# Kernel tuning notes

Measured on AMD Instinct MI355X. Metric: run time of the kernel, lower is better.

Reference implementation:

```python
import jax, jax.numpy as jnp
import numpy as np

N = 2048; E = 32768; E2 = 65536; B = 8; P = 20; M = B * P * P * P
NR = 16; SH = 9; FEAT = NR * SH; RE = 64; RH = 128; MC = 32; MH = 16; MODES = 10; CUT = 5.0


def _sh(u):
    # real spherical harmonics l=0,1,2, e3nn 'integral' normalization, on unit vectors u[...,3]
    x, y, z = u[..., 0], u[..., 1], u[..., 2]
    c0 = 0.28209479177387814  # 1/(2 sqrt(pi))
    c1 = 0.4886025119029199   # sqrt(3/(4 pi))
    l0 = jnp.full(x.shape, c0, dtype=u.dtype)
    return jnp.stack([
        l0,
        c1 * y, c1 * z, c1 * x,
        1.0925484305920792 * x * y,
        1.0925484305920792 * y * z,
        0.31539156525252005 * (3.0 * z * z - 1.0),
        1.0925484305920792 * x * z,
        0.5462742152960396 * (x * x - y * y),
    ], axis=-1)


def _gauss(r):
    # soft_one_hot_linspace(basis='gaussian', cutoff=False) * sqrt(RE)
    vals = jnp.linspace(0.0, CUT, RE)
    step = vals[1] - vals[0]
    d = (r[:, None] - vals) / step
    return jnp.exp(-d * d) / 1.12 * np.sqrt(RE)


def _norm_act(x):
    # NormActivation over irreps 16x0e + 16x1 + 16x2 (layout [16 | 16*3 | 16*5])
    s = x[:, :NR]
    v = x[:, NR:NR * 4].reshape(-1, NR, 3)
    t = x[:, NR * 4:].reshape(-1, NR, 5)
    s = s * jax.nn.sigmoid(jnp.abs(s))
    v = v * jax.nn.sigmoid(jnp.linalg.norm(v, axis=-1))[..., None]
    t = t * jax.nn.sigmoid(jnp.linalg.norm(t, axis=-1))[..., None]
    return jnp.concatenate([s, v.reshape(-1, NR * 3), t.reshape(-1, NR * 5)], axis=-1)


def _rmlp(e, m1, m2, m3):
    h = jax.nn.silu(e @ m1)
    h = jax.nn.silu(h @ m2)
    return h @ m3


def _gcn(src, dst, x, sh, emb_e, W, m1, m2, m3, n_dst, Wsc=None):
    # fully-connected tensor-product message passing: gather -> outer(feat, sh) -> GEMM
    # -> radial gate -> scatter-sum; optional self-connection
    xs = x[src]                                                    # [E, Cin]
    msg = (xs[:, :, None] * sh[:, None, :]).reshape(xs.shape[0], -1) @ W
    msg = msg * _rmlp(emb_e, m1, m2, m3)
    out = jax.ops.segment_sum(msg, dst, num_segments=n_dst)
    return out if Wsc is None else out + x @ Wsc


def _spec(x, wr, wi):
    # FNO-style 3D spectral conv on [B,P,P,P,C], low MODES kept in 4 corner blocks
    Px = x.shape[1]
    xf = jnp.fft.rfftn(x, axes=(1, 2, 3))
    w = wr + 1j * wi                                              # [4,C,C,m,m,m]
    m = MODES
    of = jnp.zeros(xf.shape, dtype=xf.dtype)
    corners = [(slice(0, m), slice(0, m)), (slice(-m, None), slice(0, m)),
               (slice(0, m), slice(-m, None)), (slice(-m, None), slice(-m, None))]
    for k, (s1, s2) in enumerate(corners):
        blk = jnp.einsum('bxyzi,ioxyz->bxyzo', xf[:, s1, s2, :m, :], w[k])
        of = of.at[:, s1, s2, :m, :].set(blk)
    return jnp.fft.irfftn(of, s=(Px, Px, Px), axes=(1, 2, 3))


def _forward(pos, cell, emb, g0_W, g0_Wsc, g0_m1, g0_m2, g0_m3,
             g12_W, g12_Wsc, g12_m1, g12_m2, g12_m3,
             a2m_W, a2m_m1, a2m_m2, a2m_m3,
             m2a_W, m2a_m1, m2a_m2, m2a_m3,
             fc0_W, fc0_b, sw_r, sw_i, pw, ff1, ff2, fc1, fc2,
             atomic_numbers, batch, edge_src, edge_dst, atom_src, mesh_dst):
    # atom-atom spherical GCN stack
    ev = pos[edge_src] - pos[edge_dst]
    el = jnp.linalg.norm(ev, axis=-1) + 1e-8
    sh_e = _sh(ev / el[:, None])
    emb_e = _gauss(el)
    x = emb[atomic_numbers]                                        # [N, NR]
    x = _gcn(edge_src, edge_dst, x, sh_e, emb_e, g0_W, g0_m1, g0_m2, g0_m3, N, g0_Wsc)
    for i in range(2):
        x = _norm_act(x)
        x = _gcn(edge_src, edge_dst, x, sh_e, emb_e, g12_W[i], g12_m1[i], g12_m2[i], g12_m3[i], N, g12_Wsc[i])
    # particle mesh positions per cell
    fr = jnp.arange(P) / P
    fg = jnp.stack(jnp.meshgrid(fr, fr, fr, indexing='ij'), axis=-1)   # [P,P,P,3]
    meshpos = jnp.einsum('xyzk,bkl->bxyzl', fg, cell).reshape(-1, 3)   # [M,3]
    # atom -> mesh conv
    ev2 = meshpos[mesh_dst] - pos[atom_src]
    el2 = jnp.linalg.norm(ev2, axis=-1) + 1e-8
    sh2 = _sh(ev2 / el2[:, None])
    emb2 = _gauss(el2)
    mf = _gcn(atom_src, mesh_dst, x, sh2, emb2, a2m_W, a2m_m1, a2m_m2, a2m_m3, M)   # [M, MC]
    mf = mf * jax.nn.sigmoid(jnp.abs(mf))                          # NormActivation on 0e
    mf = mf.reshape(B, P, P, P, MC)
    # PME / FNO mesh conv
    grid = jnp.broadcast_to(fg, (B, P, P, P, 3))
    h = jnp.concatenate([mf, grid], axis=-1) @ fc0_W + fc0_b       # lift to width MH
    for l in range(3):
        h = jax.nn.gelu(_spec(h, sw_r[l], sw_i[l]) + h @ pw[l])
        h = h + jax.nn.gelu(h @ ff1[l]) @ ff2[l]                   # using_ff branch
    h = jax.nn.gelu(h @ fc1) @ fc2                                 # [B,P,P,P,MH]
    mf2 = h.reshape(-1, MH)
    # mesh -> atom conv, per-atom energy, readout
    af = _gcn(mesh_dst, atom_src, mf2, sh2, emb2, m2a_W, m2a_m1, m2a_m2, m2a_m3, N)  # [N,1]
    return jax.ops.segment_sum(af, batch, num_segments=B)          # [B,1]


def setup_inputs():
    key = jax.random.key(0)
    ks = jax.random.split(key, 40)
    r = lambda i, shape, scale: jax.random.normal(ks[i], shape, dtype=jnp.float32) * scale
    inp = {}
    inp['pos'] = jax.random.uniform(ks[0], (N, 3), dtype=jnp.float32) * 10.0
    inp['cell'] = jnp.eye(3, dtype=jnp.float32)[None] * 10.0 + r(1, (B, 3, 3), 0.05)
    inp['atomic_numbers'] = jax.random.randint(ks[2], (N,), 1, 100)
    inp['batch'] = jnp.sort(jax.random.randint(ks[3], (N,), 0, B))
    inp['edge_src'] = jax.random.randint(ks[4], (E,), 0, N)
    inp['edge_dst'] = jax.random.randint(ks[5], (E,), 0, N)
    inp['atom_src'] = jax.random.randint(ks[6], (E2,), 0, N)
    inp['mesh_dst'] = jax.random.randint(ks[7], (E2,), 0, M)
    inp['emb'] = r(8, (100, NR), 1.0)
    inp['g0_W'] = r(9, (NR * SH, FEAT), (NR * SH) ** -0.5)
    inp['g0_Wsc'] = r(10, (NR, FEAT), NR ** -0.5)
    inp['g0_m1'] = r(11, (RE, RH), RE ** -0.5)
    inp['g0_m2'] = r(12, (RH, RH), RH ** -0.5)
    inp['g0_m3'] = r(13, (RH, FEAT), RH ** -0.5)
    inp['g12_W'] = r(14, (2, FEAT * SH, FEAT), (FEAT * SH) ** -0.5)
    inp['g12_Wsc'] = r(15, (2, FEAT, FEAT), FEAT ** -0.5)
    inp['g12_m1'] = r(16, (2, RE, RH), RE ** -0.5)
    inp['g12_m2'] = r(17, (2, RH, RH), RH ** -0.5)
    inp['g12_m3'] = r(18, (2, RH, FEAT), RH ** -0.5)
    inp['a2m_W'] = r(19, (FEAT * SH, MC), (FEAT * SH) ** -0.5)
    inp['a2m_m1'] = r(20, (RE, RH), RE ** -0.5)
    inp['a2m_m2'] = r(21, (RH, RH), RH ** -0.5)
    inp['a2m_m3'] = r(22, (RH, MC), RH ** -0.5)
    inp['m2a_W'] = r(23, (MH * SH, 1), (MH * SH) ** -0.5)
    inp['m2a_m1'] = r(24, (RE, RH), RE ** -0.5)
    inp['m2a_m2'] = r(25, (RH, RH), RH ** -0.5)
    inp['m2a_m3'] = r(26, (RH, 1), RH ** -0.5)
    inp['fc0_W'] = r(27, (MC + 3, MH), (MC + 3) ** -0.5)
    inp['fc0_b'] = jnp.zeros((MH,), dtype=jnp.float32)
    inp['sw_r'] = r(28, (3, 4, MH, MH, MODES, MODES, MODES), 1.0 / MH)
    inp['sw_i'] = r(29, (3, 4, MH, MH, MODES, MODES, MODES), 1.0 / MH)
    inp['pw'] = r(30, (3, MH, MH), MH ** -0.5)
    inp['ff1'] = r(31, (3, MH, 4 * MH), MH ** -0.5)
    inp['ff2'] = r(32, (3, 4 * MH, MH), (4 * MH) ** -0.5)
    inp['fc1'] = r(33, (MH, 128), MH ** -0.5)
    inp['fc2'] = r(34, (128, MH), 128 ** -0.5)
    return inp


def reference(pos, cell, emb, g0_W, g0_Wsc, g0_m1, g0_m2, g0_m3, g12_W, g12_Wsc, g12_m1, g12_m2, g12_m3, a2m_W, a2m_m1, a2m_m2, a2m_m3, m2a_W, m2a_m1, m2a_m2, m2a_m3, fc0_W, fc0_b, sw_r, sw_i, pw, ff1, ff2, fc1, fc2, atomic_numbers, batch, edge_src, edge_dst, atom_src, mesh_dst):
    return _forward(pos, cell, emb, g0_W, g0_Wsc, g0_m1, g0_m2, g0_m3, g12_W, g12_Wsc, g12_m1, g12_m2, g12_m3, a2m_W, a2m_m1, a2m_m2, a2m_m3, m2a_W, m2a_m1, m2a_m2, m2a_m3, fc0_W, fc0_b, sw_r, sw_i, pw, ff1, ff2, fc1, fc2, atomic_numbers, batch, edge_src, edge_dst, atom_src, mesh_dst)
```

## Files before the change

kernel.cpp:

```cpp
#include <hip/hip_runtime.h>
#include <math.h>

#define DEVI __device__ __forceinline__

namespace {

constexpr int N_  = 2048;
constexpr int E_  = 32768;
constexpr int E2_ = 65536;
constexpr int M_  = 64000;
constexpr int NT_ = 2048;
constexpr float TMAX_ = 5.5f;
constexpr float TH_ = TMAX_ / NT_;

using bf16x8 = __attribute__((ext_vector_type(8))) short;
using f32x4  = __attribute__((ext_vector_type(4))) float;

DEVI float sigm(float x)  { return 1.0f/(1.0f+expf(-x)); }
DEVI float geluf(float x) {
  float t = tanhf(0.7978845608028654f*(x + 0.044715f*x*x*x));
  return 0.5f*x*(1.0f+t);
}

DEVI unsigned short bf16rn(float x){
  unsigned u = __float_as_uint(x);
  unsigned r = u + 0x7FFFu + ((u>>16)&1u);
  return (unsigned short)(r>>16);
}
DEVI void bf16split(float x, unsigned short& h, unsigned short& l){
  h = bf16rn(x);
  float hf = __uint_as_float(((unsigned)h)<<16);
  l = bf16rn(x - hf);
}

__global__ void zero_k(float* __restrict__ p, int n){
  int i = blockIdx.x*256 + threadIdx.x;
  if (i < n) p[i] = 0.0f;
}

__global__ void meshpos_k(const float* __restrict__ cell, float* __restrict__ mp){
  int m = blockIdx.x*256 + threadIdx.x;
  if (m >= M_) return;
  int b = m/8000, r = m%8000;
  float fx = (float)(r/400)    * 0.05f;
  float fy = (float)((r/20)%20)* 0.05f;
  float fz = (float)(r%20)     * 0.05f;
  const float* c = cell + b*9;
  mp[(size_t)m*3+0] = fx*c[0] + fy*c[3] + fz*c[6];
  mp[(size_t)m*3+1] = fx*c[1] + fy*c[4] + fz*c[7];
  mp[(size_t)m*3+2] = fx*c[2] + fy*c[5] + fz*c[8];
}

__global__ void edge_geom2_k(const float* __restrict__ Ppos, const int* __restrict__ pi,
                             const float* __restrict__ Qpos, const int* __restrict__ qi,
                             float* __restrict__ sh, float* __restrict__ el_out, int nE){
  int e = blockIdx.x*256 + threadIdx.x;
  if (e >= nE) return;
  int a = pi[e], b = qi[e];
  float ex = Ppos[(size_t)a*3+0] - Qpos[(size_t)b*3+0];
  float ey = Ppos[(size_t)a*3+1] - Qpos[(size_t)b*3+1];
  float ez = Ppos[(size_t)a*3+2] - Qpos[(size_t)b*3+2];
  float el = sqrtf(ex*ex+ey*ey+ez*ez) + 1e-8f;
  el_out[e] = el;
  float x = ex/el, y = ey/el, z = ez/el;
  float* s = sh + (size_t)e*9;
  s[0] = 0.28209479177387814f;
  s[1] = 0.4886025119029199f*y;
  s[2] = 0.4886025119029199f*z;
  s[3] = 0.4886025119029199f*x;
  s[4] = 1.0925484305920792f*x*y;
  s[5] = 1.0925484305920792f*y*z;
  s[6] = 0.31539156525252005f*(3.0f*z*z-1.0f);
  s[7] = 1.0925484305920792f*x*z;
  s[8] = 0.5462742152960396f*(x*x-y*y);
}

__global__ void gather_emb_k(const float* __restrict__ emb, const int* __restrict__ an,
                             float* __restrict__ x16){
  int idx = blockIdx.x*256 + threadIdx.x;
  if (idx >= N_*16) return;
  int n = idx >> 4, f = idx & 15;
  x16[idx] = emb[(size_t)an[n]*16 + f];
}

__global__ void es_k(float* __restrict__ Es){
  int idx = blockIdx.x*256 + threadIdx.x;
  if (idx >= NT_*64) return;
  int r = idx >> 6, k = idx & 63;
  const float step = 5.0f/63.0f;
  float d = (r*TH_ - k*step)/step;
  Es[idx] = expf(-d*d)*(8.0f/1.12f);
}

DEVI float lerp_tab(const float* __restrict__ T, float el, int O, int o){
  float u = el * (1.0f/TH_);
  u = fminf(u, (float)(NT_-1));
  int i = (int)u; if (i > NT_-2) i = NT_-2;
  float f = u - (float)i;
  float t0 = T[(size_t)i*O + o];
  float t1 = T[(size_t)(i+1)*O + o];
  return t0 + f*(t1 - t0);
}

struct BG {
  const float* A[5]; const float* B[5]; float* C[5];
  int K; int Nc[5];
};
template<int ACT>
__global__ __launch_bounds__(256) void bgemm_k(BG args){
  int chain = blockIdx.z;
  const float* A = args.A[chain];
  const float* Bm = args.B[chain];
  float* C = args.C[chain];
  int K = args.K, Nc = args.Nc[chain];
  int row0 = blockIdx.y*64, col0 = blockIdx.x*64;
  if (col0 >= Nc) return;
  __shared__ float As[16][72];
  __shared__ float Bs[16][72];
  int tid = threadIdx.x;
  int tx = tid & 15, ty = tid >> 4;
  float acc[4][4] = {};
  for (int k0 = 0; k0 < K; k0 += 16) {
    { int kk = tid & 15; int mloc = tid >> 4;
      int gk = k0 + kk;
      #pragma unroll
      for (int p = 0; p < 4; ++p) {
        int m = mloc + p*16; int gm = row0 + m;
        As[kk][m] = A[(size_t)gm*K + gk];
      } }
    { int nn = tid & 63; int kl = tid >> 6;
      #pragma unroll
      for (int p = 0; p < 4; ++p) {
        int kk = kl + p*4; int gk = k0 + kk; int gn = col0 + nn;
        Bs[kk][nn] = (gn < Nc) ? Bm[(size_t)gk*Nc + gn] : 0.0f;
      } }
    __syncthreads();
    #pragma unroll
    for (int kk = 0; kk < 16; ++kk) {
      float4 a4 = *(const float4*)&As[kk][ty*4];
      float4 b4 = *(const float4*)&Bs[kk][tx*4];
      float a[4] = {a4.x,a4.y,a4.z,a4.w};
      float b[4] = {b4.x,b4.y,b4.z,b4.w};
      #pragma unroll
      for (int i=0;i<4;++i)
        #pragma unroll
        for (int j=0;j<4;++j) acc[i][j] += a[i]*b[j];
    }
    __syncthreads();
  }
  for (int i=0;i<4;++i) {
    int gm = row0 + ty*4+i;
    for (int j=0;j<4;++j) {
      int gn = col0 + tx*4+j; if (gn >= Nc) continue;
      float v = acc[i][j];
      if (ACT==1) v = v*sigm(v);
      C[(size_t)gm*Nc + gn] = v;
    }
  }
}

__global__ void convA_k(const float* __restrict__ x, unsigned short* __restrict__ hi,
                        unsigned short* __restrict__ lo, int Mr, int K, int KP){
  int idx = blockIdx.x*256 + threadIdx.x;
  if (idx >= Mr*KP) return;
  int n = idx / KP, k = idx - n*KP;
  unsigned short h = 0, l = 0;
  if (k < K) bf16split(x[(size_t)n*K + k], h, l);
  hi[idx] = h; lo[idx] = l;
}

__global__ void convT_k(const float* __restrict__ B, unsigned short* __restrict__ hi,
                        unsigned short* __restrict__ lo, int K, int Nc, int KP){
  int idx = blockIdx.x*256 + threadIdx.x;
  if (idx >= Nc*KP) return;
  int n = idx / KP, k = idx - n*KP;
  unsigned short h = 0, l = 0;
  if (k < K) bf16split(B[(size_t)k*Nc + n], h, l);
  hi[idx] = h; lo[idx] = l;
}

template<int O>
__global__ void wreshapeT_k(const float* __restrict__ W, unsigned short* __restrict__ hi,
                            unsigned short* __restrict__ lo, int F, int KP){
  int idx = blockIdx.x*256 + threadIdx.x;
  int total = 9*O*KP;
  if (idx >= total) return;
  int n = idx / KP, f = idx - n*KP;
  unsigned short h = 0, l = 0;
  if (f < F){
    int s = n / O, o = n - s*O;
    bf16split(W[(size_t)(f*9+s)*O + o], h, l);
  }
  hi[idx] = h; lo[idx] = l;
}

__global__ void normact_bf_k(const float* __restrict__ x, unsigned short* __restrict__ hi,
                             unsigned short* __restrict__ lo){
  int idx = blockIdx.x*256 + threadIdx.x;
  if (idx >= N_*16) return;
  int n = idx >> 4, r = idx & 15;
  const float* xr = x + (size_t)n*144;
  unsigned short* hr = hi + (size_t)n*160;
  unsigned short* lr = lo + (size_t)n*160;
  unsigned short h, l;
  float s = xr[r];
  bf16split(s * sigm(fabsf(s)), h, l); hr[r]=h; lr[r]=l;
  float v0 = xr[16+r*3], v1 = xr[16+r*3+1], v2 = xr[16+r*3+2];
  float gv = sigm(sqrtf(v0*v0+v1*v1+v2*v2));
  bf16split(v0*gv,h,l); hr[16+r*3]=h;   lr[16+r*3]=l;
  bf16split(v1*gv,h,l); hr[16+r*3+1]=h; lr[16+r*3+1]=l;
  bf16split(v2*gv,h,l); hr[16+r*3+2]=h; lr[16+r*3+2]=l;
  float t0=xr[64+r*5],t1=xr[64+r*5+1],t2=xr[64+r*5+2],t3=xr[64+r*5+3],t4=xr[64+r*5+4];
  float gt = sigm(sqrtf(t0*t0+t1*t1+t2*t2+t3*t3+t4*t4));
  bf16split(t0*gt,h,l); hr[64+r*5]=h;   lr[64+r*5]=l;
  bf16split(t1*gt,h,l); hr[64+r*5+1]=h; lr[64+r*5+1]=l;
  bf16split(t2*gt,h,l); hr[64+r*5+2]=h; lr[64+r*5+2]=l;
  bf16split(t3*gt,h,l); hr[64+r*5+3]=h; lr[64+r*5+3]=l;
  bf16split(t4*gt,h,l); hr[64+r*5+4]=h; lr[64+r*5+4]=l;
  hr[144+r] = 0; lr[144+r] = 0;
}

__global__ __launch_bounds__(256) void mgemm_k(const unsigned short* __restrict__ Ah,
                     const unsigned short* __restrict__ Al,
                     const unsigned short* __restrict__ BTh,
                     const unsigned short* __restrict__ Bl,
                     float* __restrict__ C, int Mr, int KP, int Nc){
  int tilesN = Nc >> 4;
  int wid = ((blockIdx.x*256 + threadIdx.x) >> 6);
  int tm = wid / tilesN, tn = wid - tm*tilesN;
  if (tm*16 >= Mr) return;
  int lane = threadIdx.x & 63;
  int l15 = lane & 15;
  int kb  = (lane >> 4) * 8;
  const unsigned short* ah = Ah + (size_t)(tm*16 + l15)*KP + kb;
  const unsigned short* al = Al + (size_t)(tm*16 + l15)*KP + kb;
  const unsigned short* bh = BTh + (size_t)(tn*16 + l15)*KP + kb;
  const unsigned short* bl = Bl  + (size_t)(tn*16 + l15)*KP + kb;
  f32x4 acc = {0.f,0.f,0.f,0.f};
  for (int k0 = 0; k0 < KP; k0 += 32) {
    bf16x8 a_h = *(const bf16x8*)(ah + k0);
    bf16x8 a_l = *(const bf16x8*)(al + k0);
    bf16x8 b_h = *(const bf16x8*)(bh + k0);
    bf16x8 b_l = *(const bf16x8*)(bl + k0);
    acc = __builtin_amdgcn_mfma_f32_16x16x32_bf16(a_h, b_h, acc, 0, 0, 0);
    acc = __builtin_amdgcn_mfma_f32_16x16x32_bf16(a_h, b_l, acc, 0, 0, 0);
    acc = __builtin_amdgcn_mfma_f32_16x16x32_bf16(a_l, b_h, acc, 0, 0, 0);
  }
  int r0 = tm*16 + (lane>>4)*4;
  int co = tn*16 + l15;
  #pragma unroll
  for (int r = 0; r < 4; ++r){
    C[(size_t)(r0+r)*Nc + co] = acc[r];
  }
}

template<int O>
__global__ void econtract_k(const float* __restrict__ Y, const int* __restrict__ src,
                            const int* __restrict__ dst, const float* __restrict__ SH,
                            const float* __restrict__ EL, const float* __restrict__ T,
                            float* __restrict__ out, int nE){
  int idx = blockIdx.x*256 + threadIdx.x;
  if (idx >= nE*O) return;
  int e = idx / O, o = idx - e*O;
  const float* sr = SH + (size_t)e*9;
  const float* yr = Y + (size_t)src[e]*(9*O) + o;
  float acc = 0.0f;
  #pragma unroll
  for (int s = 0; s < 9; ++s) acc += sr[s] * yr[s*O];
  float rv = lerp_tab(T, EL[e], O, o);
  atomicAdd(&out[(size_t)dst[e]*O + o], acc * rv);
}

__global__ void fc0_k(const float* __restrict__ mf, const float* __restrict__ Wt,
                      const float* __restrict__ bb, float* __restrict__ h){
  int idx = blockIdx.x*256 + threadIdx.x;
  if (idx >= M_*16) return;
  int m = idx >> 4, o = idx & 15;
  int r = m % 8000;
  float fx = (float)(r/400)*0.05f, fy = (float)((r/20)%20)*0.05f, fz = (float)(r%20)*0.05f;
  const float* mfr = mf + (size_t)m*32;
  float acc = bb[o];
  #pragma unroll
  for (int j=0;j<32;++j){
    float v = mfr[j];
    v = v * sigm(fabsf(v));
    acc += v*Wt[j*16+o];
  }
  acc += fx*Wt[32*16+o] + fy*Wt[33*16+o] + fz*Wt[34*16+o];
  h[idx] = acc;
}

__global__ __launch_bounds__(256) void wreorder2_k(const float* __restrict__ wr, const float* __restrict__ wi,
                          float2* __restrict__ W2){
  __shared__ float2 tile[2560];
  int l = blockIdx.y;
  const float* wrl = wr + (size_t)l*1024000;
  const float* wil = wi + (size_t)l*1024000;
  int p = blockIdx.x;
  int ky = p/20, kx = p%20;
  int corner = ((kx>=10)?1:0) + ((ky>=10)?2:0);
  int base2 = corner*256;
  int soff = (kx%10)*100 + (ky%10)*10;
  for (int t = threadIdx.x; t < 2560; t += 256){
    int chunk = t/10, kz = t - chunk*10;
    size_t src = (size_t)(base2 + chunk)*1000 + soff + kz;
    tile[kz*256 + chunk] = make_float2(wrl[src], wil[src]);
  }
  __syncthreads();
  float2* dst = W2 + (size_t)l*1024000 + (size_t)p*2560;
  for (int t = threadIdx.x; t < 2560; t += 256) dst[t] = tile[t];
}

__global__ __launch_bounds__(256) void zyfwd_k(const float* __restrict__ h, float2* __restrict__ cA){
  __shared__ float  pl[20][20][4];
  __shared__ float2 tz[20][10][4];
  __shared__ float2 tw[20];
  int tid = threadIdx.x;
  if (tid < 20){ float a = -6.283185307179586f*tid/20.0f; tw[tid] = make_float2(cosf(a), sinf(a)); }
  int bid = blockIdx.x;
  int b = bid / 80, rem = bid % 80;
  int X = rem >> 2, cg = rem & 3;
  const float* hp = h + (size_t)(b*20+X)*400*16 + cg*4;
  for (int t = tid; t < 400; t += 256) {
    int y = t/20, z = t%20;
    const float4 v = *(const float4*)(hp + (size_t)t*16);
    pl[y][z][0]=v.x; pl[y][z][1]=v.y; pl[y][z][2]=v.z; pl[y][z][3]=v.w;
  }
  __syncthreads();
  for (int t = tid; t < 800; t += 256) {
    int c = t & 3, kz = (t>>2)%10, y = t/40;
    float sr=0.0f, si=0.0f; int j=0;
    for (int z=0; z<20; ++z){
      float v = pl[y][z][c];
      float2 w = tw[j];
      sr += v*w.x; si += v*w.y;
      j += kz; if (j>=20) j-=20;
    }
    tz[y][kz][c] = make_float2(sr,si);
  }
  __syncthreads();
  for (int t = tid; t < 800; t += 256) {
    int c = t & 3, kz = (t>>2)%10, ky = t/40;
    float sr=0.0f, si=0.0f; int j=0;
    for (int y=0; y<20; ++y){
      float2 v = tz[y][kz][c];
      float2 w = tw[j];
      sr += v.x*w.x - v.y*w.y;
      si += v.x*w.y + v.y*w.x;
      j += ky; if (j>=20) j-=20;
    }
    cA[((size_t)((b*20+ky)*10+kz)*20 + X)*16 + cg*4+c] = make_float2(sr,si);
  }
}

__global__ __launch_bounds__(256) void xmix_k(const float2* __restrict__ cA, float2* __restrict__ cB,
                    const float2* __restrict__ W2){
  __shared__ float2 xin[16][20];
  __shared__ float2 Xf[20][16];
  __shared__ float2 Mx[20][16];
  __shared__ float2 twf[20], twi[20];
  int tid = threadIdx.x;
  if (tid < 20){
    float a = -6.283185307179586f*tid/20.0f;
    twf[tid] = make_float2(cosf(a), sinf(a));
    twi[tid] = make_float2(cosf(a), -sinf(a));
  }
  int bid = blockIdx.x;
  int b = bid/200, rem = bid%200;
  int ky = rem/10, kz = rem%10;
  const float2* src = cA + (size_t)((b*20+ky)*10+kz)*320;
  for (int t = tid; t < 320; t += 256){
    int x = t/16, i = t%16;
    xin[i][x] = src[t];
  }
  __syncthreads();
  for (int t = tid; t < 320; t += 256){
    int kx = t/16, i = t%16;
    float sr=0.0f, si=0.0f; int j=0;
    for (int x=0;x<20;++x){
      float2 v = xin[i][x]; float2 w = twf[j];
      sr += v.x*w.x - v.y*w.y; si += v.x*w.y + v.y*w.x;
      j += kx; if (j>=20) j-=20;
    }
    Xf[kx][i] = make_float2(sr,si);
  }
  __syncthreads();
  for (int t = tid; t < 320; t += 256){
    int kx = t/16, o = t%16;
    const float2* wp = W2 + ((size_t)(ky*20+kx)*10 + kz)*256 + o;
    float sr=0.0f, si=0.0f;
    #pragma unroll
    for (int i=0;i<16;++i){
      float2 a = Xf[kx][i];
      float2 w = wp[i*16];
      sr += a.x*w.x - a.y*w.y;
      si += a.x*w.y + a.y*w.x;
    }
    Mx[kx][o] = make_float2(sr,si);
  }
  __syncthreads();
  for (int t = tid; t < 320; t += 256){
    int x = t/16, o = t%16;
    float sr=0.0f, si=0.0f; int j=0;
    for (int kx=0;kx<20;++kx){
      float2 v = Mx[kx][o]; float2 w = twi[j];
      sr += v.x*w.x - v.y*w.y; si += v.x*w.y + v.y*w.x;
      j += x; if (j>=20) j-=20;
    }
    cB[((size_t)((b*20+x)*20+ky)*10+kz)*16 + o] = make_float2(sr,si);
  }
}

__global__ __launch_bounds__(256) void yzinv_k(const float2* __restrict__ cB, float* __restrict__ spec){
  __shared__ float2 ci[20][10][4];
  __shared__ float2 ty[20][10][4];
  __shared__ float2 twi[20];
  int tid = threadIdx.x;
  if (tid < 20){ float a = 6.283185307179586f*tid/20.0f; twi[tid] = make_float2(cosf(a), sinf(a)); }
  int bid = blockIdx.x;
  int b = bid/80, rem = bid%80;
  int X = rem>>2, cg = rem&3;
  const float2* src = cB + (size_t)(b*20+X)*200*16;
  for (int t = tid; t < 800; t += 256){
    int c = t&3, kz = (t>>2)%10, ky = t/40;
    ci[ky][kz][c] = src[(size_t)(ky*10+kz)*16 + cg*4+c];
  }
  __syncthreads();
  for (int t = tid; t < 800; t += 256){
    int c = t&3, kz = (t>>2)%10, y = t/40;
    float sr=0.0f, si=0.0f; int j=0;
    for (int ky=0;ky<20;++ky){
      float2 v = ci[ky][kz][c]; float2 w = twi[j];
      sr += v.x*w.x - v.y*w.y; si += v.x*w.y + v.y*w.x;
      j += y; if (j>=20) j-=20;
    }
    ty[y][kz][c] = make_float2(sr,si);
  }
  __syncthreads();
  float* dst = spec + (size_t)(b*20+X)*400*16 + cg*4;
  for (int t = tid; t < 1600; t += 256){
    int c = t&3, z = (t>>2)%20, y = t/80;
    float acc = ty[y][0][c].x;
    float a2 = 0.0f; int jj = 0;
    for (int kz=1; kz<10; ++kz){
      jj += z; if (jj>=20) jj-=20;
      float2 v = ty[y][kz][c]; float2 w = twi[jj];
      a2 += v.x*w.x - v.y*w.y;
    }
    acc += 2.0f*a2;
    dst[(size_t)(y*20+z)*16 + c] = acc * (1.0f/8000.0f);
  }
}

__global__ __launch_bounds__(256) void ffn3_k(const float* __restrict__ spec, const float* __restrict__ h,
                     const float* __restrict__ pw, const float* __restrict__ ff1,
                     const float* __restrict__ ff2, float* __restrict__ hout){
  __shared__ float spw[256];
  __shared__ float sf1[1024];
  __shared__ float sf2[1024];
  __shared__ float h2s[128][17];
  __shared__ float red[2][128][17];
  int tid = threadIdx.x;
  spw[tid] = pw[tid];
  for (int t = tid; t < 1024; t += 256){ sf1[t]=ff1[t]; sf2[t]=ff2[t]; }
  int rl = tid >> 1, q = tid & 1;
  int m = blockIdx.x*128 + rl;
  const float* hr = h + (size_t)m*16;
  float hl[16];
  #pragma unroll
  for (int i=0;i<16;++i) hl[i] = hr[i];
  __syncthreads();
  const float* sp = spec + (size_t)m*16;
  #pragma unroll
  for (int c=0;c<8;++c){
    int o = q*8+c;
    float acc = sp[o];
    #pragma unroll
    for (int i=0;i<16;++i) acc += hl[i]*spw[i*16+o];
    h2s[rl][o] = geluf(acc);
  }
  __syncthreads();
  float h2l[16];
  #pragma unroll
  for (int i=0;i<16;++i) h2l[i] = h2s[rl][i];
  float part[16] = {};
  for (int kk=0;kk<32;++kk){
    int k = q*32+kk;
    float a0=0.0f, a1=0.0f;
    #pragma unroll
    for (int i=0;i<8;++i){ a0 += h2l[i]*sf1[i*64+k]; a1 += h2l[8+i]*sf1[(8+i)*64+k]; }
    float tk = geluf(a0+a1);
    #pragma unroll
    for (int o=0;o<16;++o) part[o] += tk*sf2[k*16+o];
  }
  #pragma unroll
  for (int o=0;o<16;++o) red[q][rl][o] = part[o];
  __syncthreads();
  #pragma unroll
  for (int c=0;c<8;++c){
    int o = q*8+c;
    hout[(size_t)m*16+o] = h2s[rl][o] + red[0][rl][o] + red[1][rl][o];
  }
}

__global__ __launch_bounds__(256) void fctail3_k(const float* __restrict__ h, const float* __restrict__ fc1,
                        const float* __restrict__ fc2, float* __restrict__ outm){
  __shared__ float s1[2048];
  __shared__ float s2[2048];
  __shared__ float red[2][128][17];
  int tid = threadIdx.x;
  for (int t = tid; t < 2048; t += 256){ s1[t]=fc1[t]; s2[t]=fc2[t]; }
  int rl = tid >> 1, q = tid & 1;
  int m = blockIdx.x*128 + rl;
  const float* hr = h + (size_t)m*16;
  float hl[16];
  #pragma unroll
  for (int i=0;i<16;++i) hl[i] = hr[i];
  __syncthreads();
  float part[16] = {};
  for (int kk=0;kk<64;++kk){
    int k = q*64+kk;
    float a0=0.0f, a1=0.0f;
    #pragma unroll
    for (int i=0;i<8;++i){ a0 += hl[i]*s1[i*128+k]; a1 += hl[8+i]*s1[(8+i)*128+k]; }
    float tk = geluf(a0+a1);
    #pragma unroll
    for (int o=0;o<16;++o) part[o] += tk*s2[k*16+o];
  }
  #pragma unroll
  for (int o=0;o<16;++o) red[q][rl][o] = part[o];
  __syncthreads();
  #pragma unroll
  for (int c=0;c<8;++c){
    int o = q*8+c;
    outm[(size_t)m*16+o] = red[0][rl][o] + red[1][rl][o];
  }
}

__global__ void m2a_k(const float* __restrict__ mf2, const int* __restrict__ mdst,
                      const int* __restrict__ asrc, const float* __restrict__ sh2,
                      const float* __restrict__ Wt, const float* __restrict__ EL,
                      const float* __restrict__ T, float* __restrict__ af){
  int e = blockIdx.x*256 + threadIdx.x;
  if (e >= E2_) return;
  const float* xr = mf2 + (size_t)mdst[e]*16;
  const float* sr = sh2 + (size_t)e*9;
  float sh[9];
  #pragma unroll
  for (int s=0;s<9;++s) sh[s] = sr[s];
  float acc = 0.0f;
  #pragma unroll
  for (int f=0;f<16;++f) {
    float xv = xr[f];
    float dot = 0.0f;
    #pragma unroll
    for (int s=0;s<9;++s) dot += sh[s]*Wt[f*9+s];
    acc += xv*dot;
  }
  float rv = lerp_tab(T, EL[e], 1, 0);
  atomicAdd(&af[asrc[e]], acc*rv);
}

__global__ void bsum_k(const float* __restrict__ af, const int* __restrict__ batch,
                       float* __restrict__ out){
  int n = blockIdx.x*256 + threadIdx.x;
  if (n >= N_) return;
  atomicAdd(&out[batch[n]], af[n]);
}

}

extern "C" void kernel_launch(void* const* d_in, const int* in_sizes, int n_in,
                              void* d_out, int out_size, void* d_ws, size_t ws_size,
                              hipStream_t stream) {
  (void)in_sizes; (void)n_in; (void)out_size; (void)ws_size;
  const float* pos   = (const float*)d_in[0];
  const float* cell  = (const float*)d_in[1];
  const int*   an    = (const int*)d_in[2];
  const int*   batch = (const int*)d_in[3];
  const int*   esrc  = (const int*)d_in[4];
  const int*   edst  = (const int*)d_in[5];
  const int*   asrc  = (const int*)d_in[6];
  const int*   mdst  = (const int*)d_in[7];
  const float* emb   = (const float*)d_in[8];
  const float* g0_W  = (const float*)d_in[9];
  const float* g0_Wsc= (const float*)d_in[10];
  const float* g0_m1 = (const float*)d_in[11];
  const float* g0_m2 = (const float*)d_in[12];
  const float* g0_m3 = (const float*)d_in[13];
  const float* g12_W = (const float*)d_in[14];
  const float* g12_Wsc=(const float*)d_in[15];
  const float* g12_m1= (const float*)d_in[16];
  const float* g12_m2= (const float*)d_in[17];
  const float* g12_m3= (const float*)d_in[18];
  const float* a2m_W = (const float*)d_in[19];
  const float* a2m_m1= (const float*)d_in[20];
  const float* a2m_m2= (const float*)d_in[21];
  const float* a2m_m3= (const float*)d_in[22];
  const float* m2a_W = (const float*)d_in[23];
  const float* m2a_m1= (const float*)d_in[24];
  const float* m2a_m2= (const float*)d_in[25];
  const float* m2a_m3= (const float*)d_in[26];
  const float* fc0_W = (const float*)d_in[27];
  const float* fc0_b = (const float*)d_in[28];
  const float* sw_r  = (const float*)d_in[29];
  const float* sw_i  = (const float*)d_in[30];
  const float* pw    = (const float*)d_in[31];
  const float* ff1   = (const float*)d_in[32];
  const float* ff2   = (const float*)d_in[33];
  const float* fc1   = (const float*)d_in[34];
  const float* fc2   = (const float*)d_in[35];
  float* out = (float*)d_out;

  float* Wp = (float*)d_ws;
  size_t off = 0;
  auto alloc = [&](size_t n){ off = (off+3)&~(size_t)3; float* p = Wp + off; off += n; return p; };
  float* meshpos = alloc((size_t)M_*3);
  float* she   = alloc((size_t)E_*9);
  float* ELe   = alloc((size_t)E_);
  float* sh2   = alloc((size_t)E2_*9);
  float* EL2   = alloc((size_t)E2_);
  float* x16   = alloc((size_t)N_*16);
  float* xatom = alloc((size_t)N_*144);
  float* Yg    = alloc((size_t)N_*1296);
  float* mf    = alloc((size_t)M_*32);
  float* hbuf  = alloc((size_t)M_*16);
  float* htmp  = alloc((size_t)M_*16);
  float2* cA   = (float2*)alloc(1024000);
  float2* cB   = (float2*)alloc(1024000);
  float2* W2   = (float2*)alloc((size_t)3*2048000);
  float* af    = alloc((size_t)N_);
  float* Es    = alloc((size_t)NT_*64);
  float* H1g   = alloc((size_t)5*NT_*128);
  float* H2g   = alloc((size_t)5*NT_*128);
  float* T0    = alloc((size_t)NT_*144);
  float* T1    = alloc((size_t)NT_*144);
  float* T2    = alloc((size_t)NT_*144);
  float* T3    = alloc((size_t)NT_*32);
  float* T4    = alloc((size_t)NT_*1);
  unsigned short* Ah  = (unsigned short*)alloc((size_t)N_*160/2);
  unsigned short* Al  = (unsigned short*)alloc((size_t)N_*160/2);
  unsigned short* BTh = (unsigned short*)alloc((size_t)1296*160/2);
  unsigned short* BTl = (unsigned short*)alloc((size_t)1296*160/2);
  unsigned short* BWh = (unsigned short*)alloc((size_t)144*160/2);
  unsigned short* BWl = (unsigned short*)alloc((size_t)144*160/2);

  auto g1 = [](int n){ return dim3((unsigned)((n+255)/256)); };
  auto mg = [](int tiles){ return dim3((unsigned)((tiles+3)/4)); };
  const int TM = N_/16;

  zero_k<<<g1(8), 256, 0, stream>>>(out, 8);
  zero_k<<<g1(N_), 256, 0, stream>>>(af, N_);
  zero_k<<<g1(M_*32), 256, 0, stream>>>(mf, M_*32);

  meshpos_k<<<g1(M_), 256, 0, stream>>>(cell, meshpos);
  edge_geom2_k<<<g1(E_), 256, 0, stream>>>(pos, esrc, pos, edst, she, ELe, E_);
  edge_geom2_k<<<g1(E2_), 256, 0, stream>>>(meshpos, mdst, pos, asrc, sh2, EL2, E2_);
  gather_emb_k<<<g1(N_*16), 256, 0, stream>>>(emb, an, x16);

  wreorder2_k<<<dim3(400,3), 256, 0, stream>>>(sw_r, sw_i, W2);

  {
    es_k<<<g1(NT_*64), 256, 0, stream>>>(Es);
    BG l1, l2, l3;
    const float* m1s[5] = {g0_m1, g12_m1, g12_m1+(size_t)64*128, a2m_m1, m2a_m1};
    const float* m2s[5] = {g0_m2, g12_m2, g12_m2+(size_t)128*128, a2m_m2, m2a_m2};
    const float* m3s[5] = {g0_m3, g12_m3, g12_m3+(size_t)128*144, a2m_m3, m2a_m3};
    float* Ts[5] = {T0, T1, T2, T3, T4};
    int NOs[5] = {144, 144, 144, 32, 1};
    for (int c = 0; c < 5; ++c) {
      l1.A[c] = Es;                      l1.B[c] = m1s[c]; l1.C[c] = H1g + (size_t)c*NT_*128; l1.Nc[c] = 128;
      l2.A[c] = H1g + (size_t)c*NT_*128; l2.B[c] = m2s[c]; l2.C[c] = H2g + (size_t)c*NT_*128; l2.Nc[c] = 128;
      l3.A[c] = H2g + (size_t)c*NT_*128; l3.B[c] = m3s[c]; l3.C[c] = Ts[c];                   l3.Nc[c] = NOs[c];
    }
    l1.K = 64; l2.K = 128; l3.K = 128;
    bgemm_k<1><<<dim3(2, NT_/64, 5), 256, 0, stream>>>(l1);
    bgemm_k<1><<<dim3(2, NT_/64, 5), 256, 0, stream>>>(l2);
    bgemm_k<0><<<dim3(3, NT_/64, 5), 256, 0, stream>>>(l3);
  }

  convA_k<<<g1(N_*32), 256, 0, stream>>>(x16, Ah, Al, N_, 16, 32);
  wreshapeT_k<144><<<g1(9*144*32), 256, 0, stream>>>(g0_W, BTh, BTl, 16, 32);
  convT_k<<<g1(144*32), 256, 0, stream>>>(g0_Wsc, BWh, BWl, 16, 144, 32);
  mgemm_k<<<mg(TM*81), 256, 0, stream>>>(Ah, Al, BTh, BTl, Yg, N_, 32, 1296);
  mgemm_k<<<mg(TM*9),  256, 0, stream>>>(Ah, Al, BWh, BWl, xatom, N_, 32, 144);
  econtract_k<144><<<g1(E_*144), 256, 0, stream>>>(Yg, esrc, edst, she, ELe, T0, xatom, E_);

  for (int i = 0; i < 2; ++i) {
    normact_bf_k<<<g1(N_*16), 256, 0, stream>>>(xatom, Ah, Al);
    wreshapeT_k<144><<<g1(9*144*160), 256, 0, stream>>>(g12_W + (size_t)i*1296*144, BTh, BTl, 144, 160);
    convT_k<<<g1(144*160), 256, 0, stream>>>(g12_Wsc + (size_t)i*144*144, BWh, BWl, 144, 144, 160);
    mgemm_k<<<mg(TM*81), 256, 0, stream>>>(Ah, Al, BTh, BTl, Yg, N_, 160, 1296);
    mgemm_k<<<mg(TM*9),  256, 0, stream>>>(Ah, Al, BWh, BWl, xatom, N_, 160, 144);
    econtract_k<144><<<g1(E_*144), 256, 0, stream>>>(Yg, esrc, edst, she, ELe, (i==0)?T1:T2, xatom, E_);
  }

  convA_k<<<g1(N_*160), 256, 0, stream>>>(xatom, Ah, Al, N_, 144, 160);
  wreshapeT_k<32><<<g1(9*32*160), 256, 0, stream>>>(a2m_W, BTh, BTl, 144, 160);
  mgemm_k<<<mg(TM*18), 256, 0, stream>>>(Ah, Al, BTh, BTl, Yg, N_, 160, 288);
  econtract_k<32><<<g1(E2_*32), 256, 0, stream>>>(Yg, asrc, mdst, sh2, EL2, T3, mf, E2_);

  fc0_k<<<g1(M_*16), 256, 0, stream>>>(mf, fc0_W, fc0_b, hbuf);
  for (int l = 0; l < 3; ++l) {
    zyfwd_k<<<dim3(640), 256, 0, stream>>>(hbuf, cA);
    xmix_k<<<dim3(1600), 256, 0, stream>>>(cA, cB, W2 + (size_t)l*1024000);
    yzinv_k<<<dim3(640), 256, 0, stream>>>(cB, htmp);
    ffn3_k<<<dim3(500), 256, 0, stream>>>(htmp, hbuf, pw + (size_t)l*256,
                                          ff1 + (size_t)l*1024, ff2 + (size_t)l*1024, hbuf);
  }
  fctail3_k<<<dim3(500), 256, 0, stream>>>(hbuf, fc1, fc2, htmp);

  m2a_k<<<g1(E2_), 256, 0, stream>>>(htmp, mdst, asrc, sh2, m2a_W, EL2, T4, af);
  bsum_k<<<g1(N_), 256, 0, stream>>>(af, batch, out);
}
```

Baseline: 509.3 us.

## Move radial-MLP table GEMMs to batched split-bf16 MFMA kernels

Replaces the FP32 shared-memory batched GEMM for the three radial-MLP table layers with an MFMA-based batched kernel that uses hi/lo bf16 splitting (three MFMAs per step). The Gaussian basis and hidden activations are now written directly as bf16 hi/lo pairs, and the weights are pre-transposed and padded with 15 extra convTp launches. The last chain, with one output, is padded to 16 columns, so the m2a lookup now reads with stride 16. This trades a small loss of precision and extra conversion launches for matrix-core throughput on the table build.

```diff
diff --git a/kernel.cpp b/kernel.cpp
--- a/kernel.cpp
+++ b/kernel.cpp
@@ -83,13 +83,16 @@
   x16[idx] = emb[(size_t)an[n]*16 + f];
 }
 
-__global__ void es_k(float* __restrict__ Es){
+__global__ void es_bf_k(unsigned short* __restrict__ Eh, unsigned short* __restrict__ El){
   int idx = blockIdx.x*256 + threadIdx.x;
   if (idx >= NT_*64) return;
   int r = idx >> 6, k = idx & 63;
   const float step = 5.0f/63.0f;
   float d = (r*TH_ - k*step)/step;
-  Es[idx] = expf(-d*d)*(8.0f/1.12f);
+  float v = expf(-d*d)*(8.0f/1.12f);
+  unsigned short h, l;
+  bf16split(v, h, l);
+  Eh[idx] = h; El[idx] = l;
 }
 
 DEVI float lerp_tab(const float* __restrict__ T, float el, int O, int o){
@@ -102,63 +105,6 @@
   return t0 + f*(t1 - t0);
 }
 
-struct BG {
-  const float* A[5]; const float* B[5]; float* C[5];
-  int K; int Nc[5];
-};
-template<int ACT>
-__global__ __launch_bounds__(256) void bgemm_k(BG args){
-  int chain = blockIdx.z;
-  const float* A = args.A[chain];
-  const float* Bm = args.B[chain];
-  float* C = args.C[chain];
-  int K = args.K, Nc = args.Nc[chain];
-  int row0 = blockIdx.y*64, col0 = blockIdx.x*64;
-  if (col0 >= Nc) return;
-  __shared__ float As[16][72];
-  __shared__ float Bs[16][72];
-  int tid = threadIdx.x;
-  int tx = tid & 15, ty = tid >> 4;
-  float acc[4][4] = {};
-  for (int k0 = 0; k0 < K; k0 += 16) {
-    { int kk = tid & 15; int mloc = tid >> 4;
-      int gk = k0 + kk;
-      #pragma unroll
-      for (int p = 0; p < 4; ++p) {
-        int m = mloc + p*16; int gm = row0 + m;
-        As[kk][m] = A[(size_t)gm*K + gk];
-      } }
-    { int nn = tid & 63; int kl = tid >> 6;
-      #pragma unroll
-      for (int p = 0; p < 4; ++p) {
-        int kk = kl + p*4; int gk = k0 + kk; int gn = col0 + nn;
-        Bs[kk][nn] = (gn < Nc) ? Bm[(size_t)gk*Nc + gn] : 0.0f;
-      } }
-    __syncthreads();
-    #pragma unroll
-    for (int kk = 0; kk < 16; ++kk) {
-      float4 a4 = *(const float4*)&As[kk][ty*4];
-      float4 b4 = *(const float4*)&Bs[kk][tx*4];
-      float a[4] = {a4.x,a4.y,a4.z,a4.w};
-      float b[4] = {b4.x,b4.y,b4.z,b4.w};
-      #pragma unroll
-      for (int i=0;i<4;++i)
-        #pragma unroll
-        for (int j=0;j<4;++j) acc[i][j] += a[i]*b[j];
-    }
-    __syncthreads();
-  }
-  for (int i=0;i<4;++i) {
-    int gm = row0 + ty*4+i;
-    for (int j=0;j<4;++j) {
-      int gn = col0 + tx*4+j; if (gn >= Nc) continue;
-      float v = acc[i][j];
-      if (ACT==1) v = v*sigm(v);
-      C[(size_t)gm*Nc + gn] = v;
-    }
-  }
-}
-
 __global__ void convA_k(const float* __restrict__ x, unsigned short* __restrict__ hi,
                         unsigned short* __restrict__ lo, int Mr, int K, int KP){
   int idx = blockIdx.x*256 + threadIdx.x;
@@ -169,13 +115,13 @@
   hi[idx] = h; lo[idx] = l;
 }
 
-__global__ void convT_k(const float* __restrict__ B, unsigned short* __restrict__ hi,
-                        unsigned short* __restrict__ lo, int K, int Nc, int KP){
+__global__ void convTp_k(const float* __restrict__ B, unsigned short* __restrict__ hi,
+                         unsigned short* __restrict__ lo, int K, int Nc, int KP, int NcPad){
   int idx = blockIdx.x*256 + threadIdx.x;
-  if (idx >= Nc*KP) return;
+  if (idx >= NcPad*KP) return;
   int n = idx / KP, k = idx - n*KP;
   unsigned short h = 0, l = 0;
-  if (k < K) bf16split(B[(size_t)k*Nc + n], h, l);
+  if (k < K && n < Nc) bf16split(B[(size_t)k*Nc + n], h, l);
   hi[idx] = h; lo[idx] = l;
 }
 
@@ -254,6 +200,64 @@
   }
 }
 
+struct MG {
+  const unsigned short* Ah[5]; const unsigned short* Al[5];
+  const unsigned short* Bh[5]; const unsigned short* Bl[5];
+  float* Cf[5];
+  unsigned short* Ch[5]; unsigned short* Cl[5];
+  int tilesN[5]; int Nc[5]; int KP;
+};
+template<int OUTF>
+__global__ __launch_bounds__(256) void bmgemm_k(MG g, int tilesNmax){
+  int gwid = (blockIdx.x*256 + threadIdx.x) >> 6;
+  int perChain = (NT_/16)*tilesNmax;
+  int chain = gwid / perChain;
+  if (chain >= 5) return;
+  int rem = gwid - chain*perChain;
+  int tm = rem / tilesNmax, tn = rem - tm*tilesNmax;
+  if (tn >= g.tilesN[chain]) return;
+  int lane = threadIdx.x & 63;
+  int l15 = lane & 15;
+  int kb  = (lane >> 4) * 8;
+  int KP = g.KP;
+  const unsigned short* ah = g.Ah[chain] + (size_t)(tm*16 + l15)*KP + kb;
+  const unsigned short* al = g.Al[chain] + (size_t)(tm*16 + l15)*KP + kb;
+  const unsigned short* bh = g.Bh[chain] + (size_t)(tn*16 + l15)*KP + kb;
+  const unsigned short* bl = g.Bl[chain] + (size_t)(tn*16 + l15)*KP + kb;
+  f32x4 acc = {0.f,0.f,0.f,0.f};
+  for (int k0 = 0; k0 < KP; k0 += 32) {
+    bf16x8 a_h = *(const bf16x8*)(ah + k0);
+    bf16x8 a_l = *(const bf16x8*)(al + k0);
+    bf16x8 b_h = *(const bf16x8*)(bh + k0);
+    bf16x8 b_l = *(const bf16x8*)(bl + k0);
+    acc = __builtin_amdgcn_mfma_f32_16x16x32_bf16(a_h, b_h, acc, 0, 0, 0);
+    acc = __builtin_amdgcn_mfma_f32_16x16x32_bf16(a_h, b_l, acc, 0, 0, 0);
+    acc = __builtin_amdgcn_mfma_f32_16x16x32_bf16(a_l, b_h, acc, 0, 0, 0);
+  }
+  int r0 = tm*16 + (lane>>4)*4;
+  int co = tn*16 + l15;
+  if (OUTF == 0){
+    unsigned short* Ch = g.Ch[chain];
+    unsigned short* Cl = g.Cl[chain];
+    #pragma unroll
+    for (int r = 0; r < 4; ++r){
+      float v = acc[r];
+      v = v * sigm(v);
+      unsigned short h, l;
+      bf16split(v, h, l);
+      Ch[(size_t)(r0+r)*128 + co] = h;
+      Cl[(size_t)(r0+r)*128 + co] = l;
+    }
+  } else {
+    int Nc = g.Nc[chain];
+    if (co < Nc){
+      float* C = g.Cf[chain];
+      #pragma unroll
+      for (int r = 0; r < 4; ++r) C[(size_t)(r0+r)*Nc + co] = acc[r];
+    }
+  }
+}
+
 template<int O>
 __global__ void econtract_k(const float* __restrict__ Y, const int* __restrict__ src,
                             const int* __restrict__ dst, const float* __restrict__ SH,
@@ -557,7 +561,7 @@
     for (int s=0;s<9;++s) dot += sh[s]*Wt[f*9+s];
     acc += xv*dot;
   }
-  float rv = lerp_tab(T, EL[e], 1, 0);
+  float rv = lerp_tab(T, EL[e], 16, 0);
   atomicAdd(&af[asrc[e]], acc*rv);
 }
 
@@ -630,20 +634,29 @@
   float2* cB   = (float2*)alloc(1024000);
   float2* W2   = (float2*)alloc((size_t)3*2048000);
   float* af    = alloc((size_t)N_);
-  float* Es    = alloc((size_t)NT_*64);
-  float* H1g   = alloc((size_t)5*NT_*128);
-  float* H2g   = alloc((size_t)5*NT_*128);
   float* T0    = alloc((size_t)NT_*144);
   float* T1    = alloc((size_t)NT_*144);
   float* T2    = alloc((size_t)NT_*144);
   float* T3    = alloc((size_t)NT_*32);
-  float* T4    = alloc((size_t)NT_*1);
+  float* T4    = alloc((size_t)NT_*16);
   unsigned short* Ah  = (unsigned short*)alloc((size_t)N_*160/2);
   unsigned short* Al  = (unsigned short*)alloc((size_t)N_*160/2);
   unsigned short* BTh = (unsigned short*)alloc((size_t)1296*160/2);
   unsigned short* BTl = (unsigned short*)alloc((size_t)1296*160/2);
   unsigned short* BWh = (unsigned short*)alloc((size_t)144*160/2);
   unsigned short* BWl = (unsigned short*)alloc((size_t)144*160/2);
+  unsigned short* Eh  = (unsigned short*)alloc((size_t)NT_*64/2);
+  unsigned short* El  = (unsigned short*)alloc((size_t)NT_*64/2);
+  unsigned short* H1h = (unsigned short*)alloc((size_t)5*NT_*128/2);
+  unsigned short* H1l = (unsigned short*)alloc((size_t)5*NT_*128/2);
+  unsigned short* H2h = (unsigned short*)alloc((size_t)5*NT_*128/2);
+  unsigned short* H2l = (unsigned short*)alloc((size_t)5*NT_*128/2);
+  unsigned short* B1h = (unsigned short*)alloc((size_t)5*128*64/2);
+  unsigned short* B1l = (unsigned short*)alloc((size_t)5*128*64/2);
+  unsigned short* B2h = (unsigned short*)alloc((size_t)5*128*128/2);
+  unsigned short* B2l = (unsigned short*)alloc((size_t)5*128*128/2);
+  unsigned short* B3h = (unsigned short*)alloc((size_t)5*144*128/2);
+  unsigned short* B3l = (unsigned short*)alloc((size_t)5*144*128/2);
 
   auto g1 = [](int n){ return dim3((unsigned)((n+255)/256)); };
   auto mg = [](int tiles){ return dim3((unsigned)((tiles+3)/4)); };
@@ -661,27 +674,42 @@
   wreorder2_k<<<dim3(400,3), 256, 0, stream>>>(sw_r, sw_i, W2);
 
   {
-    es_k<<<g1(NT_*64), 256, 0, stream>>>(Es);
-    BG l1, l2, l3;
+    es_bf_k<<<g1(NT_*64), 256, 0, stream>>>(Eh, El);
     const float* m1s[5] = {g0_m1, g12_m1, g12_m1+(size_t)64*128, a2m_m1, m2a_m1};
     const float* m2s[5] = {g0_m2, g12_m2, g12_m2+(size_t)128*128, a2m_m2, m2a_m2};
     const float* m3s[5] = {g0_m3, g12_m3, g12_m3+(size_t)128*144, a2m_m3, m2a_m3};
+    int NOr[5]  = {144, 144, 144, 32, 1};
+    int NOp[5]  = {144, 144, 144, 32, 16};
     float* Ts[5] = {T0, T1, T2, T3, T4};
-    int NOs[5] = {144, 144, 144, 32, 1};
-    for (int c = 0; c < 5; ++c) {
-      l1.A[c] = Es;                      l1.B[c] = m1s[c]; l1.C[c] = H1g + (size_t)c*NT_*128; l1.Nc[c] = 128;
-      l2.A[c] = H1g + (size_t)c*NT_*128; l2.B[c] = m2s[c]; l2.C[c] = H2g + (size_t)c*NT_*128; l2.Nc[c] = 128;
-      l3.A[c] = H2g + (size_t)c*NT_*128; l3.B[c] = m3s[c]; l3.C[c] = Ts[c];                   l3.Nc[c] = NOs[c];
-    }
-    l1.K = 64; l2.K = 128; l3.K = 128;
-    bgemm_k<1><<<dim3(2, NT_/64, 5), 256, 0, stream>>>(l1);
-    bgemm_k<1><<<dim3(2, NT_/64, 5), 256, 0, stream>>>(l2);
-    bgemm_k<0><<<dim3(3, NT_/64, 5), 256, 0, stream>>>(l3);
+    for (int c = 0; c < 5; ++c){
+      convTp_k<<<g1(128*64), 256, 0, stream>>>(m1s[c], B1h + (size_t)c*128*64, B1l + (size_t)c*128*64, 64, 128, 64, 128);
+      convTp_k<<<g1(128*128), 256, 0, stream>>>(m2s[c], B2h + (size_t)c*128*128, B2l + (size_t)c*128*128, 128, 128, 128, 128);
+      convTp_k<<<g1(144*128), 256, 0, stream>>>(m3s[c], B3h + (size_t)c*144*128, B3l + (size_t)c*144*128, 128, NOr[c], 128, 144);
+    }
+    MG l1 = {}, l2 = {}, l3 = {};
+    for (int c = 0; c < 5; ++c){
+      l1.Ah[c]=Eh; l1.Al[c]=El;
+      l1.Bh[c]=B1h+(size_t)c*128*64; l1.Bl[c]=B1l+(size_t)c*128*64;
+      l1.Ch[c]=H1h+(size_t)c*NT_*128; l1.Cl[c]=H1l+(size_t)c*NT_*128;
+      l1.tilesN[c]=8; l1.Nc[c]=128;
+      l2.Ah[c]=H1h+(size_t)c*NT_*128; l2.Al[c]=H1l+(size_t)c*NT_*128;
+      l2.Bh[c]=B2h+(size_t)c*128*128; l2.Bl[c]=B2l+(size_t)c*128*128;
+      l2.Ch[c]=H2h+(size_t)c*NT_*128; l2.Cl[c]=H2l+(size_t)c*NT_*128;
+      l2.tilesN[c]=8; l2.Nc[c]=128;
+      l3.Ah[c]=H2h+(size_t)c*NT_*128; l3.Al[c]=H2l+(size_t)c*NT_*128;
+      l3.Bh[c]=B3h+(size_t)c*144*128; l3.Bl[c]=B3l+(size_t)c*144*128;
+      l3.Cf[c]=Ts[c];
+      l3.tilesN[c]=(NOp[c]+15)/16; l3.Nc[c]=NOp[c];
+    }
+    l1.KP=64; l2.KP=128; l3.KP=128;
+    bmgemm_k<0><<<mg(5*(NT_/16)*8), 256, 0, stream>>>(l1, 8);
+    bmgemm_k<0><<<mg(5*(NT_/16)*8), 256, 0, stream>>>(l2, 8);
+    bmgemm_k<1><<<mg(5*(NT_/16)*9), 256, 0, stream>>>(l3, 9);
   }
 
   convA_k<<<g1(N_*32), 256, 0, stream>>>(x16, Ah, Al, N_, 16, 32);
   wreshapeT_k<144><<<g1(9*144*32), 256, 0, stream>>>(g0_W, BTh, BTl, 16, 32);
-  convT_k<<<g1(144*32), 256, 0, stream>>>(g0_Wsc, BWh, BWl, 16, 144, 32);
+  convTp_k<<<g1(144*32), 256, 0, stream>>>(g0_Wsc, BWh, BWl, 16, 144, 32, 144);
   mgemm_k<<<mg(TM*81), 256, 0, stream>>>(Ah, Al, BTh, BTl, Yg, N_, 32, 1296);
   mgemm_k<<<mg(TM*9),  256, 0, stream>>>(Ah, Al, BWh, BWl, xatom, N_, 32, 144);
   econtract_k<144><<<g1(E_*144), 256, 0, stream>>>(Yg, esrc, edst, she, ELe, T0, xatom, E_);
@@ -689,7 +717,7 @@
   for (int i = 0; i < 2; ++i) {
     normact_bf_k<<<g1(N_*16), 256, 0, stream>>>(xatom, Ah, Al);
     wreshapeT_k<144><<<g1(9*144*160), 256, 0, stream>>>(g12_W + (size_t)i*1296*144, BTh, BTl, 144, 160);
-    convT_k<<<g1(144*160), 256, 0, stream>>>(g12_Wsc + (size_t)i*144*144, BWh, BWl, 144, 144, 160);
+    convTp_k<<<g1(144*160), 256, 0, stream>>>(g12_Wsc + (size_t)i*144*144, BWh, BWl, 144, 144, 160, 144);
     mgemm_k<<<mg(TM*81), 256, 0, stream>>>(Ah, Al, BTh, BTl, Yg, N_, 160, 1296);
     mgemm_k<<<mg(TM*9),  256, 0, stream>>>(Ah, Al, BWh, BWl, xatom, N_, 160, 144);
     econtract_k<144><<<g1(E_*144), 256, 0, stream>>>(Yg, esrc, edst, she, ELe, (i==0)?T1:T2, xatom, E_);
```

New measurement: 531.7 us. 1.04x slower.
